# Optimization experiments

Hardware: AMD Instinct MI355X
Metric: run time of the kernel (lower is better)

The kernel has to match this reference:

```python
import jax, jax.numpy as jnp
import numpy as np

HIDDEN = 1024

def setup_inputs() -> dict:
    key = jax.random.key(0)
    ks = jax.random.split(key, 4)
    scale = 1.0 / np.sqrt(HIDDEN)
    return {
        "X": jax.random.normal(ks[0], (4, 4096, HIDDEN), dtype=jnp.float32),
        "Wq": jax.random.normal(ks[1], (HIDDEN, HIDDEN), dtype=jnp.float32) * scale,
        "bq": jnp.zeros((HIDDEN,), dtype=jnp.float32),
        "Wk": jax.random.normal(ks[2], (HIDDEN, HIDDEN), dtype=jnp.float32) * scale,
        "bk": jnp.zeros((HIDDEN,), dtype=jnp.float32),
        "Wv": jax.random.normal(ks[3], (HIDDEN, HIDDEN), dtype=jnp.float32) * scale,
        "bv": jnp.zeros((HIDDEN,), dtype=jnp.float32),
    }

def reference(X, Wq, bq, Wk, bk, Wv, bv):
    # nn.Linear: x @ W.T + b
    Q = jnp.einsum("bsh,dh->bsd", X, Wq) + bq   # [B,S,H]
    K = jnp.einsum("bsh,dh->bsd", X, Wk) + bk
    V = jnp.einsum("bsh,dh->bsd", X, Wv) + bv
    scores = jnp.einsum("bsd,btd->bst", Q, K) / jnp.sqrt(jnp.asarray(X.shape[-1], X.dtype))  # [B,S,S]
    attn = jax.nn.softmax(scores, axis=-1)
    return jnp.einsum("bst,btd->bsd", attn, V)  # [B,S,H]
```

## Files before the change

kernel.cpp:

```cpp
#include <hip/hip_runtime.h>
#include <math.h>

#define HIDDEN 1024
#define SEQ    4096
#define BATCH  4

typedef _Float16 f16x8 __attribute__((ext_vector_type(8)));
typedef float    floatx4 __attribute__((ext_vector_type(4)));

__device__ inline void gld16(const void* g, void* l) {
    __builtin_amdgcn_global_load_lds(
        (const __attribute__((address_space(1))) unsigned int*)g,
        (__attribute__((address_space(3))) unsigned int*)l, 16, 0, 0);
}

template<int MODE>
__global__ __launch_bounds__(256)
void gemm128_kernel(const _Float16* __restrict__ A,
                    const _Float16* __restrict__ Bq,
                    const _Float16* __restrict__ Bk,
                    const _Float16* __restrict__ Bv,
                    const float* __restrict__ bq,
                    const float* __restrict__ bk,
                    const float* __restrict__ bv,
                    float alpha,
                    _Float16* __restrict__ Eo,
                    _Float16* __restrict__ Qo,
                    _Float16* __restrict__ Ko,
                    _Float16* __restrict__ Vo,
                    float* __restrict__ Lsum,
                    int K, int lda, int ldb) {
    __shared__ __align__(16) char smem[16384];
    char* sA = smem;
    char* sB = smem + 8192;

    const int tid  = threadIdx.x;
    const int lane = tid & 63;
    const int w    = tid >> 6;
    const int wm   = w & 1;
    const int wn   = w >> 1;
    const int quad = lane >> 4;
    const int l16  = lane & 15;
    const int swz  = (l16 >> 1) & 3;

    int row0, col0;
    if (MODE == 5) {
        const int n    = blockIdx.x + 24 * blockIdx.y;
        const int xcd  = n & 7;
        const int slot = n >> 3;
        const int cc   = slot % 24;
        const int rg   = xcd + 8 * (slot / 24);
        row0 = rg * 128;
        col0 = cc * 128;
    } else {
        row0 = blockIdx.y * 128;
        col0 = blockIdx.x * 128;
    }
    const int bz = blockIdx.z;

    if (MODE == 3) {
        A    += (size_t)bz * SEQ * HIDDEN;
        Bq   += (size_t)bz * SEQ * HIDDEN;
        Eo   += (size_t)bz * SEQ * SEQ;
        Lsum += (size_t)bz * SEQ;
    }

    const _Float16* Bsrc = Bq;
    int colbase = col0;
    int which = 0;
    if (MODE == 5) {
        which = col0 >> 10;
        Bsrc = (which == 0) ? Bq : (which == 1) ? Bk : Bv;
        colbase = col0 & 1023;
    }

    floatx4 acc[4][4];
    #pragma unroll
    for (int i = 0; i < 4; ++i)
        #pragma unroll
        for (int j = 0; j < 4; ++j) acc[i][j] = (floatx4){0.f, 0.f, 0.f, 0.f};

    const f16x8* pA = (const f16x8*)sA;
    const f16x8* pB = (const f16x8*)sB;

    int srow[2], scol[2];
    #pragma unroll
    for (int it = 0; it < 2; ++it) {
        const int n = tid + it * 256;
        srow[it] = n >> 2;
        scol[it] = (n & 3) ^ ((srow[it] >> 1) & 3);
    }

    for (int k0 = 0; k0 < K; k0 += 32) {
        #pragma unroll
        for (int it = 0; it < 2; ++it) {
            const int n = tid + it * 256;
            const size_t ga = (size_t)(row0 + srow[it]) * lda + (size_t)k0 + scol[it] * 8;
            const size_t gb = (size_t)(colbase + srow[it]) * ldb + (size_t)k0 + scol[it] * 8;
            gld16(A + ga, sA + n * 16);
            gld16(Bsrc + gb, sB + n * 16);
        }
        __syncthreads();

        f16x8 af[4];
        #pragma unroll
        for (int i = 0; i < 4; ++i) {
            const int r = wm * 64 + i * 16 + l16;
            af[i] = pA[r * 4 + (quad ^ swz)];
        }
        #pragma unroll
        for (int j = 0; j < 4; ++j) {
            const int c = wn * 64 + j * 16 + l16;
            const f16x8 bf = pB[c * 4 + (quad ^ swz)];
            #pragma unroll
            for (int i = 0; i < 4; ++i)
                acc[i][j] = __builtin_amdgcn_mfma_f32_16x16x32_f16(af[i], bf, acc[i][j], 0, 0, 0);
        }
        __syncthreads();
    }

    #pragma unroll
    for (int i = 0; i < 4; ++i) {
        const int r0 = row0 + wm * 64 + i * 16 + quad * 4;
        float rp[4] = {0.f, 0.f, 0.f, 0.f};

        #pragma unroll
        for (int j = 0; j < 4; ++j) {
            const int cl = (MODE == 5 ? colbase : col0) + wn * 64 + j * 16 + l16;

            if (MODE == 5) {
                const float bcol = (which == 0 ? bq : which == 1 ? bk : bv)[cl];
                if (which < 2) {
                    _Float16* O = (which == 0) ? Qo : Ko;
                    #pragma unroll
                    for (int reg = 0; reg < 4; ++reg)
                        O[(size_t)(r0 + reg) * HIDDEN + cl] =
                            (_Float16)(acc[i][j][reg] + bcol);
                } else {
                    const int bb = r0 >> 12;
                    const int s  = r0 & 4095;
                    _Float16 t[4];
                    #pragma unroll
                    for (int reg = 0; reg < 4; ++reg)
                        t[reg] = (_Float16)(acc[i][j][reg] + bcol);
                    *(uint2*)&Vo[((size_t)bb * HIDDEN + cl) * SEQ + s] = *(const uint2*)t;
                }
            } else {
                #pragma unroll
                for (int reg = 0; reg < 4; ++reg) {
                    const float v = exp2f(alpha * acc[i][j][reg] - 5.770780163555856f);
                    const _Float16 vh = (_Float16)v;
                    Eo[(size_t)(r0 + reg) * SEQ + cl] = vh;
                    rp[reg] += (float)vh;
                }
            }
        }

        if (MODE == 3) {
            #pragma unroll
            for (int off = 1; off < 16; off <<= 1)
                #pragma unroll
                for (int reg = 0; reg < 4; ++reg)
                    rp[reg] += __shfl_xor(rp[reg], off, 64);
            if (l16 == 0)
                #pragma unroll
                for (int reg = 0; reg < 4; ++reg)
                    atomicAdd(&Lsum[r0 + reg], rp[reg]);
        }
    }
}

__global__ __launch_bounds__(512, 2)
void qk8_kernel(const _Float16* __restrict__ Q,
                const _Float16* __restrict__ Kmat,
                _Float16* __restrict__ E,
                float* __restrict__ Lsum,
                float alpha) {
    __shared__ __align__(16) char smem[131072];
    char* sA = smem;
    char* sB = smem + 65536;

    const int tid  = threadIdx.x;
    const int lane = tid & 63;
    const int w    = tid >> 6;
    const int wm   = w & 1;
    const int wn   = w >> 1;
    const int quad = lane >> 4;
    const int l16  = lane & 15;
    const int swz  = (l16 >> 1) & 3;

    const int bx   = blockIdx.x;
    const int z    = blockIdx.y;
    const int wgid = (bx & 7) * 32 + (bx >> 3);
    const int row0 = (wgid >> 4) * 256;
    const int col0 = (wgid & 15) * 256;

    const _Float16* Abase = Q    + (size_t)z * SEQ * HIDDEN + (size_t)row0 * HIDDEN;
    const _Float16* Bbase = Kmat + (size_t)z * SEQ * HIDDEN + (size_t)col0 * HIDDEN;
    E    += (size_t)z * SEQ * SEQ;
    Lsum += (size_t)z * SEQ;

    const int n0 = tid, n1 = tid + 512;
    const int r0s = n0 >> 2, p0s = n0 & 3;
    const int r1s = n1 >> 2, p1s = n1 & 3;
    const int off0 = r0s * HIDDEN + (p0s ^ ((r0s >> 1) & 3)) * 8;
    const int off1 = r1s * HIDDEN + (p1s ^ ((r1s >> 1) & 3)) * 8;

    auto stage = [&](const _Float16* base, char* lh, int kt, int kh) {
        const int kb = kt * 64 + kh * 32;
        gld16(base + off0 + kb, lh + n0 * 16);
        gld16(base + off1 + kb, lh + n1 * 16);
    };

    floatx4 acc[8][4];
    #pragma unroll
    for (int i = 0; i < 8; ++i)
        #pragma unroll
        for (int j = 0; j < 4; ++j) acc[i][j] = (floatx4){0.f, 0.f, 0.f, 0.f};

    stage(Abase, sA + 0 * 16384, 0, 0);
    stage(Bbase, sB + 0 * 16384, 0, 0);
    stage(Abase, sA + 1 * 16384, 0, 1);
    stage(Bbase, sB + 1 * 16384, 0, 1);
    stage(Abase, sA + 2 * 16384, 1, 0);
    stage(Bbase, sB + 2 * 16384, 1, 0);

#define QK_PHASE(RH, KH, DO_STAGE, STAGE_EXPR, ENDBAR)                        \
  {                                                                           \
    const f16x8* pAh = (const f16x8*)(sA + (bufc * 2 + (KH)) * 16384);        \
    const f16x8* pBh = (const f16x8*)(sB + (bufc * 2 + (KH)) * 16384);        \
    f16x8 af[4], bf[4];                                                       \
    _Pragma("unroll")                                                         \
    for (int i = 0; i < 4; ++i)                                               \
      af[i] = pAh[(wm * 128 + (RH) * 64 + i * 16 + l16) * 4 + (quad ^ swz)];  \
    _Pragma("unroll")                                                         \
    for (int j = 0; j < 4; ++j)                                               \
      bf[j] = pBh[(wn * 64 + j * 16 + l16) * 4 + (quad ^ swz)];               \
    if (DO_STAGE) { STAGE_EXPR; }                                             \
    __builtin_amdgcn_s_barrier();                                             \
    asm volatile("s_waitcnt lgkmcnt(0)" ::: "memory");                        \
    __builtin_amdgcn_s_setprio(1);                                            \
    _Pragma("unroll")                                                         \
    for (int j = 0; j < 4; ++j)                                               \
      _Pragma("unroll")                                                       \
      for (int i = 0; i < 4; ++i)                                             \
        acc[(RH) * 4 + i][j] = __builtin_amdgcn_mfma_f32_16x16x32_f16(        \
            af[i], bf[j], acc[(RH) * 4 + i][j], 0, 0, 0);                     \
    __builtin_amdgcn_s_setprio(0);                                            \
    if (ENDBAR) __builtin_amdgcn_s_barrier();                                 \
  }

#define QK_TILE(T, S01, S23, LAST)                                            \
  {                                                                           \
    const int bufc = (T) & 1, bufn = bufc ^ 1;                                \
    if (LAST) asm volatile("s_waitcnt vmcnt(0)" ::: "memory");                \
    else      asm volatile("s_waitcnt vmcnt(4)" ::: "memory");                \
    __builtin_amdgcn_s_barrier();                                             \
    __builtin_amdgcn_sched_barrier(0);                                        \
    QK_PHASE(0, 0, S01, stage(Abase, sA + (bufn * 2 + 1) * 16384, (T) + 1, 1), 1) \
    QK_PHASE(1, 0, S01, stage(Bbase, sB + (bufn * 2 + 1) * 16384, (T) + 1, 1), 1) \
    QK_PHASE(0, 1, S23, stage(Abase, sA + (bufc * 2 + 0) * 16384, (T) + 2, 0), 1) \
    QK_PHASE(1, 1, S23, stage(Bbase, sB + (bufc * 2 + 0) * 16384, (T) + 2, 0), 0) \
  }

    for (int t = 0; t < 14; ++t) QK_TILE(t, 1, 1, 0)
    QK_TILE(14, 1, 0, 0)
    QK_TILE(15, 0, 0, 1)

#undef QK_TILE
#undef QK_PHASE

    #pragma unroll
    for (int i = 0; i < 8; ++i) {
        const int r0 = row0 + wm * 128 + i * 16 + quad * 4;
        float rp[4] = {0.f, 0.f, 0.f, 0.f};
        #pragma unroll
        for (int j = 0; j < 4; ++j) {
            const int cl = col0 + wn * 64 + j * 16 + l16;
            #pragma unroll
            for (int reg = 0; reg < 4; ++reg) {
                const float v = exp2f(alpha * acc[i][j][reg] - 5.770780163555856f);
                const _Float16 vh = (_Float16)v;
                E[(size_t)(r0 + reg) * SEQ + cl] = vh;
                rp[reg] += (float)vh;
            }
        }
        #pragma unroll
        for (int off = 1; off < 16; off <<= 1)
            #pragma unroll
            for (int reg = 0; reg < 4; ++reg)
                rp[reg] += __shfl_xor(rp[reg], off, 64);
        if (l16 == 0)
            #pragma unroll
            for (int reg = 0; reg < 4; ++reg)
                atomicAdd(&Lsum[r0 + reg], rp[reg]);
    }
}

__global__ __launch_bounds__(256, 2)
void gemm_pv_kernel(const _Float16* __restrict__ A,
                    const _Float16* __restrict__ B,
                    float* __restrict__ Cf,
                    const float* __restrict__ Lsum) {
    __shared__ __align__(16) char smem[24576];
    char* sA = smem;
    char* sB = smem + 8192;

    const int tid  = threadIdx.x;
    const int lane = tid & 63;
    const int w    = tid >> 6;
    const int wm   = w & 1;
    const int wn   = w >> 1;
    const int quad = lane >> 4;
    const int l16  = lane & 15;
    const int swz  = (l16 >> 1) & 3;

    const int n    = blockIdx.x;
    const int xcd  = n & 7;
    const int slot = n >> 3;
    const int c    = slot & 3;
    const int rg   = xcd + 8 * (slot >> 2);
    const int r    = rg & 31;
    const int bz   = rg >> 5;

    const int row0 = r * 128;
    const int col0 = c * 256;

    A    += (size_t)bz * SEQ * SEQ;
    B    += (size_t)bz * HIDDEN * SEQ;
    Cf   += (size_t)bz * SEQ * HIDDEN;
    Lsum += (size_t)bz * SEQ;

    floatx4 acc[4][8];
    #pragma unroll
    for (int i = 0; i < 4; ++i)
        #pragma unroll
        for (int j = 0; j < 8; ++j) acc[i][j] = (floatx4){0.f, 0.f, 0.f, 0.f};

    const f16x8* pA = (const f16x8*)sA;
    const f16x8* pB = (const f16x8*)sB;

    for (int k0 = 0; k0 < SEQ; k0 += 32) {
        #pragma unroll
        for (int it = 0; it < 2; ++it) {
            const int nc = tid + it * 256;
            const int sr = nc >> 2;
            const int sc = (nc & 3) ^ ((sr >> 1) & 3);
            gld16(A + (size_t)(row0 + sr) * SEQ + k0 + sc * 8, sA + nc * 16);
        }
        #pragma unroll
        for (int it = 0; it < 4; ++it) {
            const int nc = tid + it * 256;
            const int sr = nc >> 2;
            const int sc = (nc & 3) ^ ((sr >> 1) & 3);
            gld16(B + (size_t)(col0 + sr) * SEQ + k0 + sc * 8, sB + nc * 16);
        }
        __syncthreads();

        f16x8 af[4];
        #pragma unroll
        for (int i = 0; i < 4; ++i) {
            const int rr = wm * 64 + i * 16 + l16;
            af[i] = pA[rr * 4 + (quad ^ swz)];
        }
        #pragma unroll
        for (int j = 0; j < 8; ++j) {
            const int cc = wn * 128 + j * 16 + l16;
            const f16x8 bf = pB[cc * 4 + (quad ^ swz)];
            #pragma unroll
            for (int i = 0; i < 4; ++i)
                acc[i][j] = __builtin_amdgcn_mfma_f32_16x16x32_f16(af[i], bf, acc[i][j], 0, 0, 0);
        }
        __syncthreads();
    }

    #pragma unroll
    for (int i = 0; i < 4; ++i) {
        const int r0 = row0 + wm * 64 + i * 16 + quad * 4;
        float linv[4];
        #pragma unroll
        for (int reg = 0; reg < 4; ++reg) linv[reg] = 1.0f / Lsum[r0 + reg];
        #pragma unroll
        for (int j = 0; j < 8; ++j) {
            const int cl = col0 + wn * 128 + j * 16 + l16;
            #pragma unroll
            for (int reg = 0; reg < 4; ++reg)
                Cf[(size_t)(r0 + reg) * HIDDEN + cl] = acc[i][j][reg] * linv[reg];
        }
    }
}

__global__ __launch_bounds__(256)
void cast_x_kernel(const float* __restrict__ in, _Float16* __restrict__ out) {
    const int i = blockIdx.x * 256 + threadIdx.x;
    const float4 x = ((const float4*)in)[i];
    _Float16 h[4] = {(_Float16)x.x, (_Float16)x.y, (_Float16)x.z, (_Float16)x.w};
    ((uint2*)out)[i] = *(const uint2*)h;
}

__global__ __launch_bounds__(256)
void cast_w_kernel(const float* __restrict__ w0, const float* __restrict__ w1,
                   const float* __restrict__ w2,
                   _Float16* __restrict__ o0, _Float16* __restrict__ o1,
                   _Float16* __restrict__ o2) {
    const float* in = (blockIdx.z == 0) ? w0 : (blockIdx.z == 1) ? w1 : w2;
    _Float16* out   = (blockIdx.z == 0) ? o0 : (blockIdx.z == 1) ? o1 : o2;
    const int i = blockIdx.x * 256 + threadIdx.x;
    const float4 x = ((const float4*)in)[i];
    _Float16 h[4] = {(_Float16)x.x, (_Float16)x.y, (_Float16)x.z, (_Float16)x.w};
    ((uint2*)out)[i] = *(const uint2*)h;
}

extern "C" void kernel_launch(void* const* d_in, const int* in_sizes, int n_in,
                              void* d_out, int out_size, void* d_ws, size_t ws_size,
                              hipStream_t stream) {
    const float* X  = (const float*)d_in[0];
    const float* Wq = (const float*)d_in[1];
    const float* bq = (const float*)d_in[2];
    const float* Wk = (const float*)d_in[3];
    const float* bk = (const float*)d_in[4];
    const float* Wv = (const float*)d_in[5];
    const float* bv = (const float*)d_in[6];
    float* out = (float*)d_out;

    char* ws = (char*)d_ws;
    const size_t EB = (size_t)BATCH * SEQ * SEQ * 2;
    const size_t XB = (size_t)BATCH * SEQ * HIDDEN * 2;
    const size_t WB = (size_t)HIDDEN * HIDDEN * 2;

    _Float16* E   = (_Float16*)ws;
    _Float16* Xh  = (_Float16*)ws;
    _Float16* Wqh = (_Float16*)(ws + XB);
    _Float16* Wkh = (_Float16*)(ws + XB + WB);
    _Float16* Wvh = (_Float16*)(ws + XB + 2 * WB);
    _Float16* Qh  = (_Float16*)(ws + EB);
    _Float16* Kh  = (_Float16*)(ws + EB + XB);
    _Float16* Vt  = (_Float16*)(ws + EB + 2 * XB);
    float*    Lsum= (float*)   (ws + EB + 3 * XB);

    cast_x_kernel<<<dim3(16384), dim3(256), 0, stream>>>(X, Xh);
    cast_w_kernel<<<dim3(1024, 1, 3), dim3(256), 0, stream>>>(
        Wq, Wk, Wv, Wqh, Wkh, Wvh);

    hipMemsetAsync(Lsum, 0, (size_t)BATCH * SEQ * sizeof(float), stream);

    gemm128_kernel<5><<<dim3(24, 128, 1), dim3(256), 0, stream>>>(
        Xh, Wqh, Wkh, Wvh, bq, bk, bv, 1.0f,
        nullptr, Qh, Kh, Vt, nullptr,
        HIDDEN, HIDDEN, HIDDEN);

    const float alpha2 = (1.0f / 32.0f) * 1.4426950408889634f;
    qk8_kernel<<<dim3(256, 4), dim3(512), 0, stream>>>(Qh, Kh, E, Lsum, alpha2);

    gemm_pv_kernel<<<dim3(512), dim3(256), 0, stream>>>(E, Vt, out, Lsum);
}
```

Measured before the change: 568.7 us.

## Software-pipeline LDS fragment reads ahead of MFMA in QK^T GEMM loop

Restructures the QK^T tile loop so LDS fragment reads for the next phase are issued before the current phase's MFMAs. Register fragments are double-buffered (afA/afB, bfX/bfY), and the barrier-then-lgkmcnt(0) wait before each MFMA block is dropped in favour of finer vmcnt waits. The goal is to hide LDS read latency and cut the barriers per tile from about eight to four. The cost is extra VGPR pressure, and the hand-tuned vmcnt counts create a risk of race conditions if they are wrong.

```diff
diff --git a/kernel.cpp b/kernel.cpp
--- a/kernel.cpp
+++ b/kernel.cpp
@@ -218,57 +218,80 @@
         #pragma unroll
         for (int j = 0; j < 4; ++j) acc[i][j] = (floatx4){0.f, 0.f, 0.f, 0.f};
 
+    f16x8 afA[4], afB[4], bfX[4], bfY[4];
+
+#define RD_AF(DST, RH, KH, B_)                                                \
+  { const f16x8* pAh = (const f16x8*)(sA + ((B_) * 2 + (KH)) * 16384);        \
+    _Pragma("unroll")                                                         \
+    for (int i = 0; i < 4; ++i)                                               \
+      DST[i] = pAh[(wm * 128 + (RH) * 64 + i * 16 + l16) * 4 + (quad ^ swz)]; }
+
+#define RD_BF(DST, KH, B_)                                                    \
+  { const f16x8* pBh = (const f16x8*)(sB + ((B_) * 2 + (KH)) * 16384);        \
+    _Pragma("unroll")                                                         \
+    for (int j = 0; j < 4; ++j)                                               \
+      DST[j] = pBh[(wn * 64 + j * 16 + l16) * 4 + (quad ^ swz)]; }
+
+#define MM(RH, AF, BF)                                                        \
+  __builtin_amdgcn_sched_barrier(0);                                          \
+  __builtin_amdgcn_s_setprio(1);                                              \
+  _Pragma("unroll")                                                           \
+  for (int j = 0; j < 4; ++j)                                                 \
+    _Pragma("unroll")                                                         \
+    for (int i = 0; i < 4; ++i)                                               \
+      acc[(RH) * 4 + i][j] = __builtin_amdgcn_mfma_f32_16x16x32_f16(          \
+          AF[i], BF[j], acc[(RH) * 4 + i][j], 0, 0, 0);                       \
+  __builtin_amdgcn_s_setprio(0);
+
+#define QK_TILE(T_, S01, S23, W0S, W2S, RDNEXT)                               \
+  { const int b_ = (T_) & 1, nb_ = b_ ^ 1;                                    \
+                                                            \
+    __builtin_amdgcn_s_barrier();                                             \
+    RD_AF(afB, 1, 0, b_);                                                     \
+    if (S01) stage(Abase, sA + (nb_ * 2 + 1) * 16384, (T_) + 1, 1);           \
+    MM(0, afA, bfX)                                                           \
+    asm volatile("s_waitcnt vmcnt(" W0S ")" ::: "memory");                    \
+                                                            \
+    __builtin_amdgcn_s_barrier();                                             \
+    RD_AF(afA, 0, 1, b_);                                                     \
+    RD_BF(bfY, 1, b_);                                                        \
+    if (S01) stage(Bbase, sB + (nb_ * 2 + 1) * 16384, (T_) + 1, 1);           \
+    MM(1, afB, bfX)                                                           \
+                                                            \
+    __builtin_amdgcn_s_barrier();                                             \
+    RD_AF(afB, 1, 1, b_);                                                     \
+    if (S23) stage(Abase, sA + (b_ * 2 + 0) * 16384, (T_) + 2, 0);            \
+    MM(0, afA, bfY)                                                           \
+    if (RDNEXT) asm volatile("s_waitcnt vmcnt(" W2S ")" ::: "memory");        \
+                                                            \
+    __builtin_amdgcn_s_barrier();                                             \
+    if (RDNEXT) {                                                             \
+      RD_AF(afA, 0, 0, nb_);                                                  \
+      RD_BF(bfX, 0, nb_);                                                     \
+    }                                                                         \
+    if (S23) stage(Bbase, sB + (b_ * 2 + 0) * 16384, (T_) + 2, 0);            \
+    MM(1, afB, bfY)                                                           \
+  }
+
     stage(Abase, sA + 0 * 16384, 0, 0);
     stage(Bbase, sB + 0 * 16384, 0, 0);
     stage(Abase, sA + 1 * 16384, 0, 1);
     stage(Bbase, sB + 1 * 16384, 0, 1);
     stage(Abase, sA + 2 * 16384, 1, 0);
     stage(Bbase, sB + 2 * 16384, 1, 0);
-
-#define QK_PHASE(RH, KH, DO_STAGE, STAGE_EXPR, ENDBAR)                        \
-  {                                                                           \
-    const f16x8* pAh = (const f16x8*)(sA + (bufc * 2 + (KH)) * 16384);        \
-    const f16x8* pBh = (const f16x8*)(sB + (bufc * 2 + (KH)) * 16384);        \
-    f16x8 af[4], bf[4];                                                       \
-    _Pragma("unroll")                                                         \
-    for (int i = 0; i < 4; ++i)                                               \
-      af[i] = pAh[(wm * 128 + (RH) * 64 + i * 16 + l16) * 4 + (quad ^ swz)];  \
-    _Pragma("unroll")                                                         \
-    for (int j = 0; j < 4; ++j)                                               \
-      bf[j] = pBh[(wn * 64 + j * 16 + l16) * 4 + (quad ^ swz)];               \
-    if (DO_STAGE) { STAGE_EXPR; }                                             \
-    __builtin_amdgcn_s_barrier();                                             \
-    asm volatile("s_waitcnt lgkmcnt(0)" ::: "memory");                        \
-    __builtin_amdgcn_s_setprio(1);                                            \
-    _Pragma("unroll")                                                         \
-    for (int j = 0; j < 4; ++j)                                               \
-      _Pragma("unroll")                                                       \
-      for (int i = 0; i < 4; ++i)                                             \
-        acc[(RH) * 4 + i][j] = __builtin_amdgcn_mfma_f32_16x16x32_f16(        \
-            af[i], bf[j], acc[(RH) * 4 + i][j], 0, 0, 0);                     \
-    __builtin_amdgcn_s_setprio(0);                                            \
-    if (ENDBAR) __builtin_amdgcn_s_barrier();                                 \
-  }
-
-#define QK_TILE(T, S01, S23, LAST)                                            \
-  {                                                                           \
-    const int bufc = (T) & 1, bufn = bufc ^ 1;                                \
-    if (LAST) asm volatile("s_waitcnt vmcnt(0)" ::: "memory");                \
-    else      asm volatile("s_waitcnt vmcnt(4)" ::: "memory");                \
-    __builtin_amdgcn_s_barrier();                                             \
-    __builtin_amdgcn_sched_barrier(0);                                        \
-    QK_PHASE(0, 0, S01, stage(Abase, sA + (bufn * 2 + 1) * 16384, (T) + 1, 1), 1) \
-    QK_PHASE(1, 0, S01, stage(Bbase, sB + (bufn * 2 + 1) * 16384, (T) + 1, 1), 1) \
-    QK_PHASE(0, 1, S23, stage(Abase, sA + (bufc * 2 + 0) * 16384, (T) + 2, 0), 1) \
-    QK_PHASE(1, 1, S23, stage(Bbase, sB + (bufc * 2 + 0) * 16384, (T) + 2, 0), 0) \
-  }
-
-    for (int t = 0; t < 14; ++t) QK_TILE(t, 1, 1, 0)
-    QK_TILE(14, 1, 0, 0)
-    QK_TILE(15, 0, 0, 1)
+    asm volatile("s_waitcnt vmcnt(8)" ::: "memory");
+    __builtin_amdgcn_s_barrier();
+    RD_AF(afA, 0, 0, 0);
+    RD_BF(bfX, 0, 0);
+
+    for (int t = 0; t < 14; ++t) QK_TILE(t, 1, 1, "6", "6", 1)
+    QK_TILE(14, 1, 0, "6", "4", 1)
+    QK_TILE(15, 0, 0, "0", "0", 0)
 
 #undef QK_TILE
-#undef QK_PHASE
+#undef MM
+#undef RD_BF
+#undef RD_AF
 
     #pragma unroll
     for (int i = 0; i < 8; ++i) {
```

Result: slower. 597.1 us (+5.0%).
